# Kernel tuning notes

Hardware: AMD Instinct MI355X
Metric: run time of the kernel (lower is better)

## Reference

```python
import jax, jax.numpy as jnp
import numpy as np

B = 256          # batch of queries
H = 2048         # hidden_dim
E = 256          # embedding_dim
N = 200_000      # number of indexed items
T = 4            # num LSH tables
BITS = 8         # num_hash_bits
K = 100          # candidate_size
NEG = 1.0e6      # penalty for non-candidates (deterministic fallback)


def setup_inputs() -> dict:
    key = jax.random.key(0)
    ks = jax.random.split(key, 8)
    hidden_state = jax.random.normal(ks[0], (B, H), dtype=jnp.float32)
    # query_projection: Linear(H, E) + LayerNorm(E) + Tanh
    Wq = jax.random.normal(ks[1], (H, E), dtype=jnp.float32) / np.sqrt(H)
    bq = jnp.zeros((E,), dtype=jnp.float32)
    gamma = jnp.ones((E,), dtype=jnp.float32)
    beta = jnp.zeros((E,), dtype=jnp.float32)
    # LSH projection matrices, column-normalized as in LSHIndex.__init__
    proj = jax.random.normal(ks[2], (T, E, BITS), dtype=jnp.float32)
    proj = proj / jnp.linalg.norm(proj, axis=1, keepdims=True)
    item_emb = jax.random.normal(ks[3], (N, E), dtype=jnp.float32)
    return {
        "hidden_state": hidden_state,
        "Wq": Wq, "bq": bq, "gamma": gamma, "beta": beta,
        "proj": proj, "item_emb": item_emb,
    }


def _layernorm(x, gamma, beta, eps=1e-5):
    mu = jnp.mean(x, axis=-1, keepdims=True)
    var = jnp.mean(jnp.square(x - mu), axis=-1, keepdims=True)
    return (x - mu) * jax.lax.rsqrt(var + eps) * gamma + beta


def _hash_codes(emb, proj):
    # emb: [M, E], proj: [T, E, BITS] -> packed integer codes [T, M]
    bits = (jnp.einsum('me,teb->tmb', emb, proj) > 0).astype(jnp.int32)
    pow2 = (2 ** jnp.arange(BITS)).astype(jnp.int32)
    return jnp.einsum('tmb,b->tm', bits, pow2)


def reference(hidden_state, Wq, bq, gamma, beta, proj, item_emb):
    # query projection: Linear -> LayerNorm -> Tanh
    qv = jnp.tanh(_layernorm(hidden_state @ Wq + bq, gamma, beta))  # [B, E]

    # LSH bucketing: item is a candidate if it shares a bucket in ANY table
    item_codes = _hash_codes(item_emb, proj)          # [T, N]
    query_codes = _hash_codes(qv, proj)               # [T, B]
    match = jnp.any(query_codes[:, :, None] == item_codes[:, None, :], axis=0)  # [B, N]

    # score everything once; non-candidates penalized so they only fill in when
    # fewer than K candidates exist (deterministic analogue of the random pad)
    scores = qv @ item_emb.T                           # [B, N]
    masked = jnp.where(match, scores, scores - NEG)
    _, candidate_ids = jax.lax.top_k(masked, K)        # [B, K]
    candidate_embeddings = item_emb[candidate_ids]     # [B, K, E]
    return qv, candidate_ids, candidate_embeddings
```

## Files before the change

### kernel.cpp

```cpp
#include <hip/hip_runtime.h>
#include <math.h>

#define Bq   256
#define Hd   2048
#define Ed   256
#define Ni   200000
#define Tt   4
#define NBITS 8
#define Kk   100
#define Mm   128
#define CAPL 16384
#define CAPB 1024
#define CAP2 4096
#define NBINS 8192
#define NSLICE 64
#define ISLICE (Ni / NSLICE)
#define NXCD 8
#define SPX (NSLICE / NXCD)
#define IPB 64
#define QPB 8
#define QT  (Bq / QPB)
#define KC  16
#define KCH (Hd / KC)

#define OFF_QV64  0ull
#define OFF_QC    524288ull
#define OFF_IC    525312ull
#define OFF_CNT   1325312ull
#define OFF_CAND  1326336ull
#define OFF_LIST  103857408ull
#define OFF_PART  137411840ull

__device__ __forceinline__ bool anybyte_eq(unsigned a, unsigned b) {
  unsigned x = a ^ b;
  return ((x - 0x01010101u) & ~x & 0x80808080u) != 0u;
}
__device__ __forceinline__ unsigned fkey(float s) {
  unsigned u = __float_as_uint(s);
  return (u & 0x80000000u) ? ~u : (u | 0x80000000u);
}

__device__ __forceinline__ int find_beta(unsigned* hist, unsigned* partial_,
                                         int* sbeta, int tid, int target) {
  unsigned s = 0;
#pragma unroll 8
  for (int j = 0; j < 32; ++j) s += hist[tid * 32 + j];
  partial_[tid] = s;
  __syncthreads();
  if (tid == 0) {
    unsigned cum = 0;
    int c;
    for (c = 255; c > 0; --c) {
      if (cum + partial_[c] >= (unsigned)target) break;
      cum += partial_[c];
    }
    int b;
    for (b = c * 32 + 31; b > c * 32; --b) {
      if (cum + hist[b] >= (unsigned)target) break;
      cum += hist[b];
    }
    *sbeta = b;
  }
  __syncthreads();
  return *sbeta;
}

__global__ void __launch_bounds__(256) qproj_gemm(
    const float* __restrict__ hidden,
    const float* __restrict__ Wq,
    double* __restrict__ partial) {
  __shared__ float hs_t[KCH][QPB];
  const int e = threadIdx.x;
  const int qbase = blockIdx.x * QPB;
  const int kc = blockIdx.y;

  for (int j = e; j < QPB * KCH; j += 256) {
    int qq = j >> 7, h = j & (KCH - 1);
    hs_t[h][qq] = hidden[(size_t)(qbase + qq) * Hd + kc * KCH + h];
  }
  __syncthreads();

  double acc[QPB];
#pragma unroll
  for (int qq = 0; qq < QPB; ++qq) acc[qq] = 0.0;

  for (int h = 0; h < KCH; ++h) {
    double w = (double)Wq[(size_t)(kc * KCH + h) * Ed + e];
    float4 ha = *reinterpret_cast<const float4*>(&hs_t[h][0]);
    float4 hb = *reinterpret_cast<const float4*>(&hs_t[h][4]);
    acc[0] = fma((double)ha.x, w, acc[0]);
    acc[1] = fma((double)ha.y, w, acc[1]);
    acc[2] = fma((double)ha.z, w, acc[2]);
    acc[3] = fma((double)ha.w, w, acc[3]);
    acc[4] = fma((double)hb.x, w, acc[4]);
    acc[5] = fma((double)hb.y, w, acc[5]);
    acc[6] = fma((double)hb.z, w, acc[6]);
    acc[7] = fma((double)hb.w, w, acc[7]);
  }

#pragma unroll
  for (int qq = 0; qq < QPB; ++qq)
    partial[((size_t)kc * Bq + qbase + qq) * Ed + e] = acc[qq];
}

__global__ void qproj_fin(const double* __restrict__ partial,
                          const float* __restrict__ bq,
                          const float* __restrict__ gamma,
                          const float* __restrict__ beta,
                          const float* __restrict__ proj,
                          float* __restrict__ out_qv,
                          double* __restrict__ qv64,
                          unsigned* __restrict__ qcp,
                          unsigned* __restrict__ cnt) {
  const int q = blockIdx.x, e = threadIdx.x;
  __shared__ double red[256];
  __shared__ double qd[256];
  __shared__ double s_mu, s_rs;

  if (e == 0) cnt[q] = 0u;

  double acc = 0.0;
#pragma unroll
  for (int kc = 0; kc < KC; ++kc)
    acc += partial[((size_t)kc * Bq + q) * Ed + e];
  acc += (double)bq[e];

  red[e] = acc;
  __syncthreads();
  for (int s = 128; s > 0; s >>= 1) {
    if (e < s) red[e] += red[e + s];
    __syncthreads();
  }
  if (e == 0) s_mu = red[0] / 256.0;
  __syncthreads();
  double d = acc - s_mu;
  red[e] = d * d;
  __syncthreads();
  for (int s = 128; s > 0; s >>= 1) {
    if (e < s) red[e] += red[e + s];
    __syncthreads();
  }
  if (e == 0) s_rs = 1.0 / sqrt(red[0] / 256.0 + 1e-5);
  __syncthreads();

  double y = (acc - s_mu) * s_rs * (double)gamma[e] + (double)beta[e];
  double t = tanh(y);
  out_qv[(size_t)q * Ed + e] = (float)t;
  qv64[(size_t)q * Ed + e] = t;
  qd[e] = t;
  __syncthreads();

  double dot = 0.0;
  if (e < 32) {
    const int tt = e >> 3, b = e & 7;
    const float* pp = proj + (size_t)tt * Ed * NBITS + b;
#pragma unroll 4
    for (int ee = 0; ee < Ed; ++ee)
      dot = fma(qd[ee], (double)pp[(size_t)ee * NBITS], dot);
  }
  unsigned long long mask = __ballot(e < 32 && dot > 0.0);
  if (e == 0) qcp[q] = (unsigned)mask;
}

__global__ void __launch_bounds__(256) icode_kernel(
    const float* __restrict__ item,
    const float* __restrict__ proj,
    unsigned* __restrict__ icodes) {
  __shared__ float ts[IPB * 65];
  __shared__ unsigned icode_s[IPB];
  const int tid = threadIdx.x;
  const int base = blockIdx.x * IPB;
  const int il = tid & 63;
  const int t = __builtin_amdgcn_readfirstlane(tid >> 6);
  const float* pt = proj + (size_t)t * (Ed * NBITS);

  if (tid < IPB) icode_s[tid] = 0u;

  float acc[8];
#pragma unroll
  for (int b = 0; b < 8; ++b) acc[b] = 0.0f;

  for (int c = 0; c < 4; ++c) {
    __syncthreads();
#pragma unroll
    for (int rep = 0; rep < 16; ++rep) {
      const int fi = rep * 256 + tid;
      const int row = fi >> 6, e = fi & 63;
      ts[row * 65 + e] = item[(size_t)(base + row) * Ed + c * 64 + e];
    }
    __syncthreads();

#pragma unroll 8
    for (int e = 0; e < 64; ++e) {
      const float av = ts[il * 65 + e];
      const float4 pa = *reinterpret_cast<const float4*>(&pt[(size_t)(c * 64 + e) * 8]);
      const float4 pb = *reinterpret_cast<const float4*>(&pt[(size_t)(c * 64 + e) * 8 + 4]);
      acc[0] = fmaf(av, pa.x, acc[0]);
      acc[1] = fmaf(av, pa.y, acc[1]);
      acc[2] = fmaf(av, pa.z, acc[2]);
      acc[3] = fmaf(av, pa.w, acc[3]);
      acc[4] = fmaf(av, pb.x, acc[4]);
      acc[5] = fmaf(av, pb.y, acc[5]);
      acc[6] = fmaf(av, pb.z, acc[6]);
      acc[7] = fmaf(av, pb.w, acc[7]);
    }
  }

  unsigned byte = 0, bl = 0;
#pragma unroll
  for (int b = 0; b < 8; ++b) {
    byte |= (acc[b] > 0.0f ? 1u : 0u) << b;
    bl |= (fabsf(acc[b]) < 2e-4f ? 1u : 0u) << b;
  }

  if (bl) {
    const int gi = base + il;
    const float* er = item + (size_t)gi * Ed;
    while (bl) {
      const int b = __builtin_ctz(bl);
      bl &= bl - 1;
      const float* pp = pt + b;
      double a = 0.0;
      for (int e2 = 0; e2 < Ed; ++e2)
        a = fma((double)er[e2], (double)pp[(size_t)e2 * NBITS], a);
      if (a > 0.0) byte |= 1u << b; else byte &= ~(1u << b);
    }
  }

  atomicOr(&icode_s[il], byte << (8 * t));
  __syncthreads();
  if (tid < IPB) icodes[base + tid] = icode_s[tid];
}

__global__ void __launch_bounds__(256) score_kernel(
    const float* __restrict__ qvf,
    const float* __restrict__ item,
    const unsigned* __restrict__ icodes,
    const unsigned* __restrict__ qcp,
    unsigned* __restrict__ cnt,
    unsigned long long* __restrict__ list) {
  __shared__ unsigned long long buf[CAPB];
  __shared__ int lcnt;
  __shared__ unsigned sbase;

  const int tid = threadIdx.x;
  const int lin = blockIdx.x;
  const int xcd = lin & (NXCD - 1);
  const int rank = lin >> 3;
  const int sl = xcd * SPX + (rank >> 8);
  const int q = rank & 255;
  const int l = tid & 63, wid = tid >> 6;
  const int k = tid & 7;
  const int gg = tid >> 3;

  if (tid == 0) lcnt = 0;
  const unsigned qc = qcp[q];

  float4 qv[8];
#pragma unroll
  for (int c = 0; c < 8; ++c)
    qv[c] = *reinterpret_cast<const float4*>(&qvf[(size_t)q * Ed + (c * 8 + k) * 4]);
  __syncthreads();

  const int i0 = sl * ISLICE, i1 = i0 + ISLICE;
  for (int bse = i0 + wid * 64; bse < i1; bse += 256) {
    const int i = bse + l;
    bool m = (i < i1) && anybyte_eq(qc, icodes[i]);
    unsigned long long mask = __ballot(m);
    if (mask) {
      int base_ = 0;
      if (l == 0) base_ = atomicAdd(&lcnt, __popcll(mask));
      base_ = __shfl(base_, 0);
      if (m) {
        int rnk = __popcll(mask & ((1ull << l) - 1ull));
        int pos = base_ + rnk;
        if (pos < CAPB) buf[pos] = (unsigned long long)(unsigned)i;
      }
    }
  }
  __syncthreads();

  if (lcnt > CAPB) {
    if (tid == 0) atomicAdd(&cnt[q], (unsigned)(CAPL + 1));
    return;
  }
  const int nl = lcnt;

  for (int b = gg; b < nl; b += 64) {
    const int b1 = b + 32;
    const bool has1 = (b1 < nl);
    const int id0 = (int)(unsigned)buf[b];
    const int id1 = has1 ? (int)(unsigned)buf[b1] : id0;
    const float* r0 = item + (size_t)id0 * Ed;
    const float* r1 = item + (size_t)id1 * Ed;
    float p0 = 0.0f, p1 = 0.0f;
#pragma unroll
    for (int c = 0; c < 8; ++c) {
      const float4 e0 = *reinterpret_cast<const float4*>(&r0[(c * 8 + k) * 4]);
      const float4 e1 = *reinterpret_cast<const float4*>(&r1[(c * 8 + k) * 4]);
      p0 = fmaf(e0.x, qv[c].x, fmaf(e0.y, qv[c].y,
           fmaf(e0.z, qv[c].z, fmaf(e0.w, qv[c].w, p0))));
      p1 = fmaf(e1.x, qv[c].x, fmaf(e1.y, qv[c].y,
           fmaf(e1.z, qv[c].z, fmaf(e1.w, qv[c].w, p1))));
    }
#pragma unroll
    for (int off = 1; off < 8; off <<= 1) {
      p0 += __shfl_xor(p0, off);
      p1 += __shfl_xor(p1, off);
    }
    if (k == 0) {
      buf[b] = ((unsigned long long)fkey(p0) << 32) | (unsigned)(~(unsigned)id0);
      if (has1)
        buf[b1] = ((unsigned long long)fkey(p1) << 32) | (unsigned)(~(unsigned)id1);
    }
  }
  __syncthreads();

  if (tid == 0) sbase = atomicAdd(&cnt[q], (unsigned)nl);
  __syncthreads();
  const unsigned bp = sbase;
  for (int j = tid; j < nl; j += 256) {
    unsigned p = bp + (unsigned)j;
    if (p < CAPL) list[(size_t)q * CAPL + p] = buf[j];
  }
}

__global__ void fallback_kernel(const double* __restrict__ qv64,
                                const float* __restrict__ item,
                                const unsigned* __restrict__ qcp,
                                const unsigned* __restrict__ icodes,
                                unsigned* __restrict__ cnt,
                                unsigned long long* __restrict__ list) {
  const int q = blockIdx.x, tid = threadIdx.x;
  unsigned c = cnt[q];
  if (c >= (unsigned)Mm && c <= (unsigned)CAPL) return;

  __shared__ unsigned hist[NBINS];
  __shared__ float qf[256];
  __shared__ unsigned partial_[256];
  __shared__ int sbeta, scnt;

  qf[tid] = (float)qv64[(size_t)q * Ed + tid];
  for (int j = tid; j < NBINS; j += 256) hist[j] = 0u;
  if (tid == 0) scnt = 0;
  __syncthreads();

  const unsigned qc = qcp[q];
  for (int i = tid; i < Ni; i += 256) {
    float s = 0.0f;
    const float* er = item + (size_t)i * Ed;
    for (int e = 0; e < Ed; ++e) s = fmaf(qf[e], er[e], s);
    if (!anybyte_eq(qc, icodes[i])) s -= 1.0e6f;
    atomicAdd(&hist[fkey(s) >> 19], 1u);
  }
  __syncthreads();

  int beta = find_beta(hist, partial_, &sbeta, tid, Mm);
  __syncthreads();

  for (int i = tid; i < Ni; i += 256) {
    float s = 0.0f;
    const float* er = item + (size_t)i * Ed;
    for (int e = 0; e < Ed; ++e) s = fmaf(qf[e], er[e], s);
    if (!anybyte_eq(qc, icodes[i])) s -= 1.0e6f;
    unsigned kk = fkey(s);
    if ((int)(kk >> 19) >= beta) {
      int pos = atomicAdd(&scnt, 1);
      if (pos < CAPL)
        list[(size_t)q * CAPL + pos] =
            ((unsigned long long)kk << 32) | (unsigned)(~(unsigned)i);
    }
  }
  __syncthreads();
  if (tid == 0) cnt[q] = (unsigned)(scnt < CAPL ? scnt : CAPL);
}

__global__ void select_kernel(const unsigned long long* __restrict__ list,
                              const unsigned* __restrict__ cnt,
                              unsigned* __restrict__ cand) {
  __shared__ unsigned long long buf[CAP2];
  __shared__ unsigned partial_[256];
  __shared__ int sbeta, scnt;
  unsigned* hist = reinterpret_cast<unsigned*>(buf);

  const int q = blockIdx.x, tid = threadIdx.x;
  const unsigned long long* src = list + (size_t)q * CAPL;
  const int count = min((int)cnt[q], CAPL);

  for (int j = tid; j < NBINS; j += 256) hist[j] = 0u;
  if (tid == 0) scnt = 0;
  __syncthreads();

  for (int i = tid; i < count; i += 256)
    atomicAdd(&hist[(unsigned)(src[i] >> 32) >> 19], 1u);
  __syncthreads();

  int beta = find_beta(hist, partial_, &sbeta, tid, Mm);
  __syncthreads();

  for (int i = tid; i < count; i += 256) {
    unsigned long long v = src[i];
    if ((int)((unsigned)(v >> 32) >> 19) >= beta) {
      int pos = atomicAdd(&scnt, 1);
      if (pos < CAP2) buf[pos] = v;
    }
  }
  __syncthreads();

  int sc = min(scnt, CAP2);
  int n = Mm;
  while (n < sc) n <<= 1;
  for (int j = tid; j < n; j += 256)
    if (j >= sc) buf[j] = 0ull;
  __syncthreads();

  for (int k2 = 2; k2 <= n; k2 <<= 1) {
    for (int j = k2 >> 1; j > 0; j >>= 1) {
      for (int i = tid; i < n; i += 256) {
        int p = i ^ j;
        if (p > i) {
          bool up = ((i & k2) == 0);
          unsigned long long a = buf[i], b = buf[p];
          if ((a < b) == up) { buf[i] = b; buf[p] = a; }
        }
      }
      __syncthreads();
    }
  }

  if (tid < Mm)
    cand[q * Mm + tid] = ~(unsigned)(buf[tid] & 0xFFFFFFFFull);
}

__global__ void rerank_kernel(const double* __restrict__ qv64,
                              const float* __restrict__ item,
                              const unsigned* __restrict__ qcp,
                              const unsigned* __restrict__ icodes,
                              const unsigned* __restrict__ cand,
                              float* __restrict__ out_ids,
                              float* __restrict__ out_emb) {
  const int q = blockIdx.x, tid = threadIdx.x;
  const int l = tid & 63, w = tid >> 6;
  __shared__ double qr[Ed];
  __shared__ double sc[Mm];
  __shared__ int sid[Mm];

  qr[tid] = qv64[(size_t)q * Ed + tid];
  if (tid < Mm) {
    int id = (int)cand[q * Mm + tid];
    if (id < 0 || id >= Ni) id = 0;
    sid[tid] = id;
  }
  __syncthreads();

  const unsigned qc = qcp[q];
  for (int cc = 0; cc < Mm / 4; ++cc) {
    const int ci = w * (Mm / 4) + cc;
    const int id = sid[ci];
    float4 ev = *reinterpret_cast<const float4*>(&item[(size_t)id * Ed + l * 4]);
    double p = fma((double)ev.x, qr[l * 4 + 0],
               fma((double)ev.y, qr[l * 4 + 1],
               fma((double)ev.z, qr[l * 4 + 2],
                   (double)ev.w * qr[l * 4 + 3])));
#pragma unroll
    for (int off = 32; off > 0; off >>= 1) p += __shfl_down(p, off);
    if (l == 0) {
      double s = p;
      if (!anybyte_eq(qc, icodes[id])) s -= 1.0e6;
      sc[ci] = s;
    }
  }
  __syncthreads();

  for (int k2 = 2; k2 <= Mm; k2 <<= 1) {
    for (int j = k2 >> 1; j > 0; j >>= 1) {
      for (int i = tid; i < Mm; i += 256) {
        int p = i ^ j;
        if (p > i) {
          bool up = ((i & k2) == 0);
          double sa = sc[i], sb = sc[p];
          int ia = sid[i], ib = sid[p];
          bool aAfterB = (sa < sb) || (sa == sb && ia > ib);
          if (aAfterB == up) {
            sc[i] = sb; sc[p] = sa;
            sid[i] = ib; sid[p] = ia;
          }
        }
      }
      __syncthreads();
    }
  }

  if (tid < Kk) out_ids[q * Kk + tid] = (float)sid[tid];
  for (int f = tid; f < Kk * 64; f += 256) {
    int r = f >> 6, c4 = f & 63;
    *reinterpret_cast<float4*>(&out_emb[((size_t)q * Kk + r) * Ed + c4 * 4]) =
        *reinterpret_cast<const float4*>(&item[(size_t)sid[r] * Ed + c4 * 4]);
  }
}

extern "C" void kernel_launch(void* const* d_in, const int* in_sizes, int n_in,
                              void* d_out, int out_size, void* d_ws, size_t ws_size,
                              hipStream_t stream) {
  const float* hidden = (const float*)d_in[0];
  const float* Wq     = (const float*)d_in[1];
  const float* bq     = (const float*)d_in[2];
  const float* gamma  = (const float*)d_in[3];
  const float* beta   = (const float*)d_in[4];
  const float* proj   = (const float*)d_in[5];
  const float* item   = (const float*)d_in[6];

  float* out = (float*)d_out;
  char* ws = (char*)d_ws;
  double*             qv64 = (double*)(ws + OFF_QV64);
  unsigned*           qcp  = (unsigned*)(ws + OFF_QC);
  unsigned*           ic   = (unsigned*)(ws + OFF_IC);
  unsigned*           cnt  = (unsigned*)(ws + OFF_CNT);
  unsigned*           cand = (unsigned*)(ws + OFF_CAND);
  unsigned long long* list = (unsigned long long*)(ws + OFF_LIST);
  double*             part = (double*)(ws + OFF_PART);

  qproj_gemm<<<dim3(QT, KC), dim3(256), 0, stream>>>(hidden, Wq, part);
  icode_kernel<<<dim3(Ni / IPB), dim3(256), 0, stream>>>(item, proj, ic);
  qproj_fin<<<dim3(Bq), dim3(256), 0, stream>>>(part, bq, gamma, beta, proj,
                                                out, qv64, qcp, cnt);
  score_kernel<<<dim3(Bq * NSLICE), dim3(256), 0, stream>>>(out, item, ic, qcp, cnt, list);
  fallback_kernel<<<dim3(Bq), dim3(256), 0, stream>>>(qv64, item, qcp, ic, cnt, list);
  select_kernel<<<dim3(Bq), dim3(256), 0, stream>>>(list, cnt, cand);
  rerank_kernel<<<dim3(Bq), dim3(256), 0, stream>>>(
      qv64, item, qcp, ic, cand,
      out + (size_t)Bq * Ed, out + (size_t)Bq * Ed + (size_t)Bq * Kk);
}
```

Measured before the change: 245.4 us.

## Fuse kernels and score four queries per block sharing item code loads

Merges the query-projection GEMM and item-hash kernels into one launch. It also merges the fallback, select and rerank kernels into a single per-query kernel, which drops the intermediate candidate buffer. The score kernel now handles four queries per block, so each icode load is reused across queries, and a per-entry query tag lets matches from all four share one buffer. This cuts launch count and redundant icode reads, at the cost of more shared memory, a fallback path that now runs inside the select kernel, and per-entry atomics for the output scatter.

```diff
diff --git a/kernel.cpp b/kernel.cpp
--- a/kernel.cpp
+++ b/kernel.cpp
@@ -10,13 +10,14 @@
 #define Kk   100
 #define Mm   128
 #define CAPL 16384
-#define CAPB 1024
+#define CAPB2 512
 #define CAP2 4096
 #define NBINS 8192
 #define NSLICE 64
 #define ISLICE (Ni / NSLICE)
 #define NXCD 8
 #define SPX (NSLICE / NXCD)
+#define QPS 4
 #define IPB 64
 #define QPB 8
 #define QT  (Bq / QPB)
@@ -27,7 +28,6 @@
 #define OFF_QC    524288ull
 #define OFF_IC    525312ull
 #define OFF_CNT   1325312ull
-#define OFF_CAND  1326336ull
 #define OFF_LIST  103857408ull
 #define OFF_PART  137411840ull
 
@@ -65,42 +65,115 @@
   return *sbeta;
 }
 
-__global__ void __launch_bounds__(256) qproj_gemm(
+__global__ void __launch_bounds__(256) qp_icode_kernel(
     const float* __restrict__ hidden,
     const float* __restrict__ Wq,
-    double* __restrict__ partial) {
-  __shared__ float hs_t[KCH][QPB];
-  const int e = threadIdx.x;
-  const int qbase = blockIdx.x * QPB;
-  const int kc = blockIdx.y;
-
-  for (int j = e; j < QPB * KCH; j += 256) {
-    int qq = j >> 7, h = j & (KCH - 1);
-    hs_t[h][qq] = hidden[(size_t)(qbase + qq) * Hd + kc * KCH + h];
-  }
-  __syncthreads();
-
-  double acc[QPB];
-#pragma unroll
-  for (int qq = 0; qq < QPB; ++qq) acc[qq] = 0.0;
-
-  for (int h = 0; h < KCH; ++h) {
-    double w = (double)Wq[(size_t)(kc * KCH + h) * Ed + e];
-    float4 ha = *reinterpret_cast<const float4*>(&hs_t[h][0]);
-    float4 hb = *reinterpret_cast<const float4*>(&hs_t[h][4]);
-    acc[0] = fma((double)ha.x, w, acc[0]);
-    acc[1] = fma((double)ha.y, w, acc[1]);
-    acc[2] = fma((double)ha.z, w, acc[2]);
-    acc[3] = fma((double)ha.w, w, acc[3]);
-    acc[4] = fma((double)hb.x, w, acc[4]);
-    acc[5] = fma((double)hb.y, w, acc[5]);
-    acc[6] = fma((double)hb.z, w, acc[6]);
-    acc[7] = fma((double)hb.w, w, acc[7]);
-  }
-
-#pragma unroll
-  for (int qq = 0; qq < QPB; ++qq)
-    partial[((size_t)kc * Bq + qbase + qq) * Ed + e] = acc[qq];
+    double* __restrict__ partial,
+    const float* __restrict__ item,
+    const float* __restrict__ proj,
+    unsigned* __restrict__ icodes) {
+  __shared__ float smem[IPB * 65];
+  __shared__ unsigned icode_s[IPB];
+  const int blk = blockIdx.x;
+  const int tid = threadIdx.x;
+
+  if (blk < QT * KC) {
+    float (*hs_t)[QPB] = reinterpret_cast<float (*)[QPB]>(smem);
+    const int e = tid;
+    const int qbase = (blk & (QT - 1)) * QPB;
+    const int kc = blk >> 5;
+
+    for (int j = e; j < QPB * KCH; j += 256) {
+      int qq = j >> 7, h = j & (KCH - 1);
+      hs_t[h][qq] = hidden[(size_t)(qbase + qq) * Hd + kc * KCH + h];
+    }
+    __syncthreads();
+
+    double acc[QPB];
+#pragma unroll
+    for (int qq = 0; qq < QPB; ++qq) acc[qq] = 0.0;
+
+    for (int h = 0; h < KCH; ++h) {
+      double w = (double)Wq[(size_t)(kc * KCH + h) * Ed + e];
+      float4 ha = *reinterpret_cast<const float4*>(&hs_t[h][0]);
+      float4 hb = *reinterpret_cast<const float4*>(&hs_t[h][4]);
+      acc[0] = fma((double)ha.x, w, acc[0]);
+      acc[1] = fma((double)ha.y, w, acc[1]);
+      acc[2] = fma((double)ha.z, w, acc[2]);
+      acc[3] = fma((double)ha.w, w, acc[3]);
+      acc[4] = fma((double)hb.x, w, acc[4]);
+      acc[5] = fma((double)hb.y, w, acc[5]);
+      acc[6] = fma((double)hb.z, w, acc[6]);
+      acc[7] = fma((double)hb.w, w, acc[7]);
+    }
+
+#pragma unroll
+    for (int qq = 0; qq < QPB; ++qq)
+      partial[((size_t)kc * Bq + qbase + qq) * Ed + e] = acc[qq];
+    return;
+  }
+
+  const int base = (blk - QT * KC) * IPB;
+  const int il = tid & 63;
+  const int t = __builtin_amdgcn_readfirstlane(tid >> 6);
+  const float* pt = proj + (size_t)t * (Ed * NBITS);
+
+  if (tid < IPB) icode_s[tid] = 0u;
+
+  float acc[8];
+#pragma unroll
+  for (int b = 0; b < 8; ++b) acc[b] = 0.0f;
+
+  for (int c = 0; c < 4; ++c) {
+    __syncthreads();
+#pragma unroll
+    for (int rep = 0; rep < 16; ++rep) {
+      const int fi = rep * 256 + tid;
+      const int row = fi >> 6, e = fi & 63;
+      smem[row * 65 + e] = item[(size_t)(base + row) * Ed + c * 64 + e];
+    }
+    __syncthreads();
+
+#pragma unroll 8
+    for (int e = 0; e < 64; ++e) {
+      const float av = smem[il * 65 + e];
+      const float4 pa = *reinterpret_cast<const float4*>(&pt[(size_t)(c * 64 + e) * 8]);
+      const float4 pb = *reinterpret_cast<const float4*>(&pt[(size_t)(c * 64 + e) * 8 + 4]);
+      acc[0] = fmaf(av, pa.x, acc[0]);
+      acc[1] = fmaf(av, pa.y, acc[1]);
+      acc[2] = fmaf(av, pa.z, acc[2]);
+      acc[3] = fmaf(av, pa.w, acc[3]);
+      acc[4] = fmaf(av, pb.x, acc[4]);
+      acc[5] = fmaf(av, pb.y, acc[5]);
+      acc[6] = fmaf(av, pb.z, acc[6]);
+      acc[7] = fmaf(av, pb.w, acc[7]);
+    }
+  }
+
+  unsigned byte = 0, bl = 0;
+#pragma unroll
+  for (int b = 0; b < 8; ++b) {
+    byte |= (acc[b] > 0.0f ? 1u : 0u) << b;
+    bl |= (fabsf(acc[b]) < 2e-4f ? 1u : 0u) << b;
+  }
+
+  if (bl) {
+    const int gi = base + il;
+    const float* er = item + (size_t)gi * Ed;
+    while (bl) {
+      const int b = __builtin_ctz(bl);
+      bl &= bl - 1;
+      const float* pp = pt + b;
+      double a = 0.0;
+      for (int e2 = 0; e2 < Ed; ++e2)
+        a = fma((double)er[e2], (double)pp[(size_t)e2 * NBITS], a);
+      if (a > 0.0) byte |= 1u << b; else byte &= ~(1u << b);
+    }
+  }
+
+  atomicOr(&icode_s[il], byte << (8 * t));
+  __syncthreads();
+  if (tid < IPB) icodes[base + tid] = icode_s[tid];
 }
 
 __global__ void qproj_fin(const double* __restrict__ partial,
@@ -162,76 +235,6 @@
   if (e == 0) qcp[q] = (unsigned)mask;
 }
 
-__global__ void __launch_bounds__(256) icode_kernel(
-    const float* __restrict__ item,
-    const float* __restrict__ proj,
-    unsigned* __restrict__ icodes) {
-  __shared__ float ts[IPB * 65];
-  __shared__ unsigned icode_s[IPB];
-  const int tid = threadIdx.x;
-  const int base = blockIdx.x * IPB;
-  const int il = tid & 63;
-  const int t = __builtin_amdgcn_readfirstlane(tid >> 6);
-  const float* pt = proj + (size_t)t * (Ed * NBITS);
-
-  if (tid < IPB) icode_s[tid] = 0u;
-
-  float acc[8];
-#pragma unroll
-  for (int b = 0; b < 8; ++b) acc[b] = 0.0f;
-
-  for (int c = 0; c < 4; ++c) {
-    __syncthreads();
-#pragma unroll
-    for (int rep = 0; rep < 16; ++rep) {
-      const int fi = rep * 256 + tid;
-      const int row = fi >> 6, e = fi & 63;
-      ts[row * 65 + e] = item[(size_t)(base + row) * Ed + c * 64 + e];
-    }
-    __syncthreads();
-
-#pragma unroll 8
-    for (int e = 0; e < 64; ++e) {
-      const float av = ts[il * 65 + e];
-      const float4 pa = *reinterpret_cast<const float4*>(&pt[(size_t)(c * 64 + e) * 8]);
-      const float4 pb = *reinterpret_cast<const float4*>(&pt[(size_t)(c * 64 + e) * 8 + 4]);
-      acc[0] = fmaf(av, pa.x, acc[0]);
-      acc[1] = fmaf(av, pa.y, acc[1]);
-      acc[2] = fmaf(av, pa.z, acc[2]);
-      acc[3] = fmaf(av, pa.w, acc[3]);
-      acc[4] = fmaf(av, pb.x, acc[4]);
-      acc[5] = fmaf(av, pb.y, acc[5]);
-      acc[6] = fmaf(av, pb.z, acc[6]);
-      acc[7] = fmaf(av, pb.w, acc[7]);
-    }
-  }
-
-  unsigned byte = 0, bl = 0;
-#pragma unroll
-  for (int b = 0; b < 8; ++b) {
-    byte |= (acc[b] > 0.0f ? 1u : 0u) << b;
-    bl |= (fabsf(acc[b]) < 2e-4f ? 1u : 0u) << b;
-  }
-
-  if (bl) {
-    const int gi = base + il;
-    const float* er = item + (size_t)gi * Ed;
-    while (bl) {
-      const int b = __builtin_ctz(bl);
-      bl &= bl - 1;
-      const float* pp = pt + b;
-      double a = 0.0;
-      for (int e2 = 0; e2 < Ed; ++e2)
-        a = fma((double)er[e2], (double)pp[(size_t)e2 * NBITS], a);
-      if (a > 0.0) byte |= 1u << b; else byte &= ~(1u << b);
-    }
-  }
-
-  atomicOr(&icode_s[il], byte << (8 * t));
-  __syncthreads();
-  if (tid < IPB) icodes[base + tid] = icode_s[tid];
-}
-
 __global__ void __launch_bounds__(256) score_kernel(
     const float* __restrict__ qvf,
     const float* __restrict__ item,
@@ -239,49 +242,64 @@
     const unsigned* __restrict__ qcp,
     unsigned* __restrict__ cnt,
     unsigned long long* __restrict__ list) {
-  __shared__ unsigned long long buf[CAPB];
+  __shared__ unsigned long long buf[QPS * CAPB2];
+  __shared__ unsigned char qibuf[QPS * CAPB2];
+  __shared__ float qvs[QPS][Ed];
   __shared__ int lcnt;
-  __shared__ unsigned sbase;
+  __shared__ unsigned ccnt[QPS], fcnt[QPS], sbase_s[QPS];
 
   const int tid = threadIdx.x;
   const int lin = blockIdx.x;
   const int xcd = lin & (NXCD - 1);
   const int rank = lin >> 3;
-  const int sl = xcd * SPX + (rank >> 8);
-  const int q = rank & 255;
+  const int sl = xcd * SPX + (rank >> 6);
+  const int q0 = (rank & 63) * QPS;
   const int l = tid & 63, wid = tid >> 6;
   const int k = tid & 7;
   const int gg = tid >> 3;
 
   if (tid == 0) lcnt = 0;
-  const unsigned qc = qcp[q];
-
-  float4 qv[8];
-#pragma unroll
-  for (int c = 0; c < 8; ++c)
-    qv[c] = *reinterpret_cast<const float4*>(&qvf[(size_t)q * Ed + (c * 8 + k) * 4]);
+  if (tid < QPS) { ccnt[tid] = 0u; fcnt[tid] = 0u; }
+
+  unsigned qc[QPS];
+#pragma unroll
+  for (int qi = 0; qi < QPS; ++qi) qc[qi] = qcp[q0 + qi];
+
+  for (int j = tid; j < QPS * (Ed / 4); j += 256) {
+    int qi = j >> 6, c4 = j & 63;
+    *reinterpret_cast<float4*>(&qvs[qi][c4 * 4]) =
+        *reinterpret_cast<const float4*>(&qvf[(size_t)(q0 + qi) * Ed + c4 * 4]);
+  }
   __syncthreads();
 
   const int i0 = sl * ISLICE, i1 = i0 + ISLICE;
   for (int bse = i0 + wid * 64; bse < i1; bse += 256) {
     const int i = bse + l;
-    bool m = (i < i1) && anybyte_eq(qc, icodes[i]);
-    unsigned long long mask = __ballot(m);
-    if (mask) {
-      int base_ = 0;
-      if (l == 0) base_ = atomicAdd(&lcnt, __popcll(mask));
-      base_ = __shfl(base_, 0);
-      if (m) {
-        int rnk = __popcll(mask & ((1ull << l) - 1ull));
-        int pos = base_ + rnk;
-        if (pos < CAPB) buf[pos] = (unsigned long long)(unsigned)i;
+    const bool iv = (i < i1);
+    const unsigned code = iv ? icodes[i] : 0u;
+#pragma unroll
+    for (int qi = 0; qi < QPS; ++qi) {
+      bool m = iv && anybyte_eq(qc[qi], code);
+      unsigned long long mask = __ballot(m);
+      if (mask) {
+        int base_ = 0;
+        if (l == 0) base_ = atomicAdd(&lcnt, __popcll(mask));
+        base_ = __shfl(base_, 0);
+        if (m) {
+          int rnk = __popcll(mask & ((1ull << l) - 1ull));
+          int pos = base_ + rnk;
+          if (pos < QPS * CAPB2) {
+            buf[pos] = (unsigned long long)(unsigned)i;
+            qibuf[pos] = (unsigned char)qi;
+          }
+        }
       }
     }
   }
   __syncthreads();
 
-  if (lcnt > CAPB) {
-    if (tid == 0) atomicAdd(&cnt[q], (unsigned)(CAPL + 1));
+  if (lcnt > QPS * CAPB2) {
+    if (tid < QPS) atomicAdd(&cnt[q0 + tid], (unsigned)(CAPL + 1));
     return;
   }
   const int nl = lcnt;
@@ -290,18 +308,22 @@
     const int b1 = b + 32;
     const bool has1 = (b1 < nl);
     const int id0 = (int)(unsigned)buf[b];
+    const int qi0 = qibuf[b];
     const int id1 = has1 ? (int)(unsigned)buf[b1] : id0;
+    const int qi1 = has1 ? qibuf[b1] : qi0;
     const float* r0 = item + (size_t)id0 * Ed;
     const float* r1 = item + (size_t)id1 * Ed;
     float p0 = 0.0f, p1 = 0.0f;
 #pragma unroll
     for (int c = 0; c < 8; ++c) {
       const float4 e0 = *reinterpret_cast<const float4*>(&r0[(c * 8 + k) * 4]);
+      const float4 qa = *reinterpret_cast<const float4*>(&qvs[qi0][(c * 8 + k) * 4]);
       const float4 e1 = *reinterpret_cast<const float4*>(&r1[(c * 8 + k) * 4]);
-      p0 = fmaf(e0.x, qv[c].x, fmaf(e0.y, qv[c].y,
-           fmaf(e0.z, qv[c].z, fmaf(e0.w, qv[c].w, p0))));
-      p1 = fmaf(e1.x, qv[c].x, fmaf(e1.y, qv[c].y,
-           fmaf(e1.z, qv[c].z, fmaf(e1.w, qv[c].w, p1))));
+      const float4 qb = *reinterpret_cast<const float4*>(&qvs[qi1][(c * 8 + k) * 4]);
+      p0 = fmaf(e0.x, qa.x, fmaf(e0.y, qa.y,
+           fmaf(e0.z, qa.z, fmaf(e0.w, qa.w, p0))));
+      p1 = fmaf(e1.x, qb.x, fmaf(e1.y, qb.y,
+           fmaf(e1.z, qb.z, fmaf(e1.w, qb.w, p1))));
     }
 #pragma unroll
     for (int off = 1; off < 8; off <<= 1) {
@@ -316,76 +338,79 @@
   }
   __syncthreads();
 
-  if (tid == 0) sbase = atomicAdd(&cnt[q], (unsigned)nl);
-  __syncthreads();
-  const unsigned bp = sbase;
+  for (int j = tid; j < nl; j += 256) atomicAdd(&ccnt[qibuf[j]], 1u);
+  __syncthreads();
+  if (tid < QPS) sbase_s[tid] = atomicAdd(&cnt[q0 + tid], ccnt[tid]);
+  __syncthreads();
   for (int j = tid; j < nl; j += 256) {
-    unsigned p = bp + (unsigned)j;
-    if (p < CAPL) list[(size_t)q * CAPL + p] = buf[j];
-  }
-}
-
-__global__ void fallback_kernel(const double* __restrict__ qv64,
-                                const float* __restrict__ item,
-                                const unsigned* __restrict__ qcp,
-                                const unsigned* __restrict__ icodes,
-                                unsigned* __restrict__ cnt,
-                                unsigned long long* __restrict__ list) {
-  const int q = blockIdx.x, tid = threadIdx.x;
-  unsigned c = cnt[q];
-  if (c >= (unsigned)Mm && c <= (unsigned)CAPL) return;
-
-  __shared__ unsigned hist[NBINS];
-  __shared__ float qf[256];
-  __shared__ unsigned partial_[256];
-  __shared__ int sbeta, scnt;
-
-  qf[tid] = (float)qv64[(size_t)q * Ed + tid];
-  for (int j = tid; j < NBINS; j += 256) hist[j] = 0u;
-  if (tid == 0) scnt = 0;
-  __syncthreads();
-
-  const unsigned qc = qcp[q];
-  for (int i = tid; i < Ni; i += 256) {
-    float s = 0.0f;
-    const float* er = item + (size_t)i * Ed;
-    for (int e = 0; e < Ed; ++e) s = fmaf(qf[e], er[e], s);
-    if (!anybyte_eq(qc, icodes[i])) s -= 1.0e6f;
-    atomicAdd(&hist[fkey(s) >> 19], 1u);
-  }
-  __syncthreads();
-
-  int beta = find_beta(hist, partial_, &sbeta, tid, Mm);
-  __syncthreads();
-
-  for (int i = tid; i < Ni; i += 256) {
-    float s = 0.0f;
-    const float* er = item + (size_t)i * Ed;
-    for (int e = 0; e < Ed; ++e) s = fmaf(qf[e], er[e], s);
-    if (!anybyte_eq(qc, icodes[i])) s -= 1.0e6f;
-    unsigned kk = fkey(s);
-    if ((int)(kk >> 19) >= beta) {
-      int pos = atomicAdd(&scnt, 1);
-      if (pos < CAPL)
-        list[(size_t)q * CAPL + pos] =
-            ((unsigned long long)kk << 32) | (unsigned)(~(unsigned)i);
-    }
-  }
-  __syncthreads();
-  if (tid == 0) cnt[q] = (unsigned)(scnt < CAPL ? scnt : CAPL);
-}
-
-__global__ void select_kernel(const unsigned long long* __restrict__ list,
-                              const unsigned* __restrict__ cnt,
-                              unsigned* __restrict__ cand) {
+    const int qi = qibuf[j];
+    unsigned pos = sbase_s[qi] + atomicAdd(&fcnt[qi], 1u);
+    if (pos < CAPL) list[(size_t)(q0 + qi) * CAPL + pos] = buf[j];
+  }
+}
+
+__global__ void selrerank_kernel(unsigned long long* __restrict__ list,
+                                 const unsigned* __restrict__ cnt,
+                                 const double* __restrict__ qv64,
+                                 const float* __restrict__ item,
+                                 const unsigned* __restrict__ qcp,
+                                 const unsigned* __restrict__ icodes,
+                                 float* __restrict__ out_ids,
+                                 float* __restrict__ out_emb) {
   __shared__ unsigned long long buf[CAP2];
   __shared__ unsigned partial_[256];
   __shared__ int sbeta, scnt;
+  __shared__ double qr[Ed];
+  __shared__ float qf[256];
+  __shared__ double sc[Mm];
+  __shared__ int sid[Mm];
   unsigned* hist = reinterpret_cast<unsigned*>(buf);
 
   const int q = blockIdx.x, tid = threadIdx.x;
-  const unsigned long long* src = list + (size_t)q * CAPL;
-  const int count = min((int)cnt[q], CAPL);
+  const int l = tid & 63, w = tid >> 6;
+  unsigned long long* src = list + (size_t)q * CAPL;
+  const unsigned qc = qcp[q];
+
+  double qv_e = qv64[(size_t)q * Ed + tid];
+  qr[tid] = qv_e;
+  qf[tid] = (float)qv_e;
+  __syncthreads();
+
+  int count = (int)min(cnt[q], (unsigned)(CAPL + 256));
+
+  if (count < Mm || count > CAPL) {
+    for (int j = tid; j < NBINS; j += 256) hist[j] = 0u;
+    if (tid == 0) scnt = 0;
+    __syncthreads();
+
+    for (int i = tid; i < Ni; i += 256) {
+      float s = 0.0f;
+      const float* er = item + (size_t)i * Ed;
+      for (int e = 0; e < Ed; ++e) s = fmaf(qf[e], er[e], s);
+      if (!anybyte_eq(qc, icodes[i])) s -= 1.0e6f;
+      atomicAdd(&hist[fkey(s) >> 19], 1u);
+    }
+    __syncthreads();
+
+    int beta = find_beta(hist, partial_, &sbeta, tid, Mm);
+    __syncthreads();
+
+    for (int i = tid; i < Ni; i += 256) {
+      float s = 0.0f;
+      const float* er = item + (size_t)i * Ed;
+      for (int e = 0; e < Ed; ++e) s = fmaf(qf[e], er[e], s);
+      if (!anybyte_eq(qc, icodes[i])) s -= 1.0e6f;
+      unsigned kk = fkey(s);
+      if ((int)(kk >> 19) >= beta) {
+        int pos = atomicAdd(&scnt, 1);
+        if (pos < CAPL)
+          src[pos] = ((unsigned long long)kk << 32) | (unsigned)(~(unsigned)i);
+      }
+    }
+    __syncthreads();
+    count = min(scnt, CAPL);
+    __syncthreads();
+  }
 
   for (int j = tid; j < NBINS; j += 256) hist[j] = 0u;
   if (tid == 0) scnt = 0;
@@ -407,11 +432,11 @@
   }
   __syncthreads();
 
-  int sc = min(scnt, CAP2);
+  int scv = min(scnt, CAP2);
   int n = Mm;
-  while (n < sc) n <<= 1;
+  while (n < scv) n <<= 1;
   for (int j = tid; j < n; j += 256)
-    if (j >= sc) buf[j] = 0ull;
+    if (j >= scv) buf[j] = 0ull;
   __syncthreads();
 
   for (int k2 = 2; k2 <= n; k2 <<= 1) {
@@ -428,32 +453,13 @@
     }
   }
 
-  if (tid < Mm)
-    cand[q * Mm + tid] = ~(unsigned)(buf[tid] & 0xFFFFFFFFull);
-}
-
-__global__ void rerank_kernel(const double* __restrict__ qv64,
-                              const float* __restrict__ item,
-                              const unsigned* __restrict__ qcp,
-                              const unsigned* __restrict__ icodes,
-                              const unsigned* __restrict__ cand,
-                              float* __restrict__ out_ids,
-                              float* __restrict__ out_emb) {
-  const int q = blockIdx.x, tid = threadIdx.x;
-  const int l = tid & 63, w = tid >> 6;
-  __shared__ double qr[Ed];
-  __shared__ double sc[Mm];
-  __shared__ int sid[Mm];
-
-  qr[tid] = qv64[(size_t)q * Ed + tid];
   if (tid < Mm) {
-    int id = (int)cand[q * Mm + tid];
+    int id = (int)(~(unsigned)(buf[tid] & 0xFFFFFFFFull));
     if (id < 0 || id >= Ni) id = 0;
     sid[tid] = id;
   }
   __syncthreads();
 
-  const unsigned qc = qcp[q];
   for (int cc = 0; cc < Mm / 4; ++cc) {
     const int ci = w * (Mm / 4) + cc;
     const int id = sid[ci];
@@ -516,18 +522,16 @@
   unsigned*           qcp  = (unsigned*)(ws + OFF_QC);
   unsigned*           ic   = (unsigned*)(ws + OFF_IC);
   unsigned*           cnt  = (unsigned*)(ws + OFF_CNT);
-  unsigned*           cand = (unsigned*)(ws + OFF_CAND);
   unsigned long long* list = (unsigned long long*)(ws + OFF_LIST);
   double*             part = (double*)(ws + OFF_PART);
 
-  qproj_gemm<<<dim3(QT, KC), dim3(256), 0, stream>>>(hidden, Wq, part);
-  icode_kernel<<<dim3(Ni / IPB), dim3(256), 0, stream>>>(item, proj, ic);
+  qp_icode_kernel<<<dim3(QT * KC + Ni / IPB), dim3(256), 0, stream>>>(
+      hidden, Wq, part, item, proj, ic);
   qproj_fin<<<dim3(Bq), dim3(256), 0, stream>>>(part, bq, gamma, beta, proj,
                                                 out, qv64, qcp, cnt);
-  score_kernel<<<dim3(Bq * NSLICE), dim3(256), 0, stream>>>(out, item, ic, qcp, cnt, list);
-  fallback_kernel<<<dim3(Bq), dim3(256), 0, stream>>>(qv64, item, qcp, ic, cnt, list);
-  select_kernel<<<dim3(Bq), dim3(256), 0, stream>>>(list, cnt, cand);
-  rerank_kernel<<<dim3(Bq), dim3(256), 0, stream>>>(
-      qv64, item, qcp, ic, cand,
+  score_kernel<<<dim3(NSLICE * (Bq / QPS)), dim3(256), 0, stream>>>(
+      out, item, ic, qcp, cnt, list);
+  selrerank_kernel<<<dim3(Bq), dim3(256), 0, stream>>>(
+      list, cnt, qv64, item, qcp, ic,
       out + (size_t)Bq * Ed, out + (size_t)Bq * Ed + (size_t)Bq * Kk);
 }
```

New measurement: 203.1 us. 1.21x faster.
